# Performance work log

Hardware: AMD Instinct MI355X
Metric: run time of the kernel (lower is better)

Reference implementation:

```python
import jax, jax.numpy as jnp
import numpy as np

L = 2        # layer_depth
H = 128      # rnn_size (== embedding dim)
V = 50257    # vocab_size
B = 100      # batch_size
T = 50       # seq_length


def setup_inputs() -> dict:
    key = jax.random.key(0)
    ks = jax.random.split(key, 8)
    inp = {
        'input_data': jax.random.randint(ks[0], (B, T), 0, V, dtype=jnp.int32),
        # embedding ~ U(-0.08, 0.08) as in the original
        'embedding': jax.random.uniform(ks[1], (V, H), jnp.float32, -0.08, 0.08),
        # per-layer GRU params; input dim == H for every layer
        'gate_k': jax.random.normal(ks[2], (L, 2 * H, 2 * H), jnp.float32) * 0.05,
        'gate_b': jnp.ones((L, 2 * H), jnp.float32),  # TF GRUCell gate bias init = 1.0
        'cand_k': jax.random.normal(ks[3], (L, 2 * H, H), jnp.float32) * 0.05,
        'cand_b': jnp.zeros((L, H), jnp.float32),
        'softmax_w': jax.random.normal(ks[4], (V, H), jnp.float32) * 0.05,
        'softmax_b': jnp.zeros((V,), jnp.float32),
    }
    return inp


def _gru_scan(x_bth, gate_k, gate_b, cand_k, cand_b):
    # x_bth: [B, T, H] embedded inputs. Stacked L-layer GRU, TF GRUCell math:
    #   r,u = sigmoid([x,h] @ Wg + bg);  c = tanh([x, r*h] @ Wc + bc)
    #   h' = u*h + (1-u)*c
    x_tbh = jnp.swapaxes(x_bth, 0, 1)  # [T, B, H]
    h0 = jnp.zeros((L, x_bth.shape[0], H), x_bth.dtype)

    def step(hs, x_t):
        inp = x_t
        new_hs = []
        for l in range(L):
            h = hs[l]
            g = jax.nn.sigmoid(jnp.concatenate([inp, h], -1) @ gate_k[l] + gate_b[l])
            r, u = g[:, :H], g[:, H:]
            c = jnp.tanh(jnp.concatenate([inp, r * h], -1) @ cand_k[l] + cand_b[l])
            h_new = u * h + (1.0 - u) * c
            new_hs.append(h_new)
            inp = h_new
        return jnp.stack(new_hs), inp

    final_state, out_tbh = jax.lax.scan(step, h0, x_tbh)
    return jnp.swapaxes(out_tbh, 0, 1), final_state  # [B, T, H], [L, B, H]


def reference(input_data, embedding, gate_k, gate_b, cand_k, cand_b, softmax_w, softmax_b):
    x = embedding[input_data]                                   # [B, T, H]
    out, _ = _gru_scan(x, gate_k, gate_b, cand_k, cand_b)       # [B, T, H]
    out = out.reshape(-1, H)                                    # [B*T, H]
    logits = out @ softmax_w.T + softmax_b                      # [B*T, V]
    probs = jax.nn.softmax(logits, axis=-1)
    return logits, probs
```

## Files before the change

kernel.cpp:

```cpp
#include <hip/hip_runtime.h>
#include <hip/hip_bf16.h>
#include <math.h>

#define GL 2
#define GH 128
#define GH2 256
#define GV 50257
#define GB 100
#define GT 50
#define GM 5000
#define NT 393
#define MT 40

typedef __attribute__((ext_vector_type(4))) float f32x4;
typedef __attribute__((ext_vector_type(8))) short bf16x8;

__global__ __launch_bounds__(1024) void gru_kernel(
    const int* __restrict__ tok,
    const float* __restrict__ emb,
    const float* __restrict__ gate_k,
    const float* __restrict__ gate_b,
    const float* __restrict__ cand_k,
    const float* __restrict__ cand_b,
    float* __restrict__ out)
{
    const int b = blockIdx.x;
    const int tid = threadIdx.x;

    __shared__ float xin[GH2];
    __shared__ float hs[2][GH];
    __shared__ float g[GH2];
    __shared__ float gpart[4][GH2];
    __shared__ float cpart[8][GH];

    if (tid < GH) { hs[0][tid] = 0.f; hs[1][tid] = 0.f; }
    __syncthreads();

    for (int t = 0; t < GT; ++t) {
        const int token = tok[b * GT + t];
        if (tid < GH) xin[tid] = emb[(size_t)token * GH + tid];

        for (int l = 0; l < GL; ++l) {
            if (tid >= GH && tid < GH2) xin[tid] = hs[l][tid - GH];
            __syncthreads();

            {
                const int j  = tid & 255;
                const int t4 = tid >> 8;
                const float* gcol = gate_k + (size_t)l * GH2 * GH2 + (size_t)(t4 * 64) * GH2 + j;
                const float* xv = xin + t4 * 64;
                float acc = 0.f;
                #pragma unroll 16
                for (int i = 0; i < 64; ++i) acc += xv[i] * gcol[(size_t)i * GH2];
                gpart[t4][j] = acc;
            }
            __syncthreads();
            if (tid < GH2) {
                float s = gpart[0][tid] + gpart[1][tid] + gpart[2][tid] + gpart[3][tid]
                        + gate_b[l * GH2 + tid];
                g[tid] = 1.f / (1.f + expf(-s));
            }
            __syncthreads();
            if (tid >= GH && tid < GH2) xin[tid] = g[tid - GH] * hs[l][tid - GH];
            __syncthreads();

            {
                const int j  = tid & 127;
                const int t8 = tid >> 7;
                const float* ccol = cand_k + (size_t)l * GH2 * GH + (size_t)(t8 * 32) * GH + j;
                const float* xv = xin + t8 * 32;
                float acc = 0.f;
                #pragma unroll 16
                for (int i = 0; i < 32; ++i) acc += xv[i] * ccol[(size_t)i * GH];
                cpart[t8][j] = acc;
            }
            __syncthreads();
            if (tid < GH) {
                float csum = 0.f;
                #pragma unroll
                for (int p = 0; p < 8; ++p) csum += cpart[p][tid];
                const float c = tanhf(csum + cand_b[l * GH + tid]);
                const float u = g[GH + tid];
                const float hn = u * hs[l][tid] + (1.f - u) * c;
                hs[l][tid] = hn;
                xin[tid] = hn;
                if (l == GL - 1) out[(size_t)(b * GT + t) * GH + tid] = hn;
            }
            __syncthreads();
        }
    }
}

__device__ __forceinline__ unsigned short f2bf(float x) {
    union { float f; unsigned u; } c; c.f = x;
    unsigned r = c.u + 0x7FFFu + ((c.u >> 16) & 1u);
    return (unsigned short)(r >> 16);
}
__device__ __forceinline__ float bf2f(unsigned short b) {
    union { unsigned u; float f; } c; c.u = ((unsigned)b) << 16; return c.f;
}

__global__ __launch_bounds__(256) void prep_kernel(
    const float* __restrict__ src, unsigned short* __restrict__ dst,
    int ntiles, int nrows)
{
    const int idx = blockIdx.x * 256 + threadIdx.x;
    if (idx >= ntiles * 4 * 128) return;
    const int r    = idx & 127;
    const int c    = idx >> 7;
    const int cs   = c & 3;
    const int tile = c >> 2;
    int row = tile * 128 + r; if (row > nrows - 1) row = nrows - 1;
    const float* s = src + (size_t)row * GH + (cs & 1) * 64;
    unsigned short* d = dst + (size_t)c * 8192 + r * 64;
    const bool lo = (cs >= 2);
    const int rx = r & 7;

    #pragma unroll
    for (int gq = 0; gq < 8; ++gq) {
        float x[8];
        *(float4*)(x)     = *(const float4*)(s + gq * 8);
        *(float4*)(x + 4) = *(const float4*)(s + gq * 8 + 4);
        unsigned u[4];
        #pragma unroll
        for (int q = 0; q < 4; ++q) {
            const float a0 = x[q * 2], a1 = x[q * 2 + 1];
            const unsigned short hi0 = f2bf(a0), hi1 = f2bf(a1);
            unsigned short h0, h1;
            if (lo) { h0 = f2bf(a0 - bf2f(hi0)); h1 = f2bf(a1 - bf2f(hi1)); }
            else    { h0 = hi0; h1 = hi1; }
            u[q] = (unsigned)h0 | ((unsigned)h1 << 16);
        }
        *(uint4*)(d + (size_t)((gq ^ rx) * 8)) = *(const uint4*)u;
    }
}

__global__ __launch_bounds__(256) void mfma_logits_kernel(
    const unsigned short* __restrict__ Ap, const unsigned short* __restrict__ Wp,
    const float* __restrict__ bias,
    float* __restrict__ logits, float* __restrict__ pmax, float* __restrict__ psum)
{
    __shared__ unsigned short ldsA[8192];
    __shared__ unsigned short ldsW[8192];
    __shared__ float sM[2][128];
    __shared__ float sS[2][128];

    const int bt  = blockIdx.x;
    const int bm  = blockIdx.y;
    const int tid = threadIdx.x;
    const int wid  = tid >> 6;
    const int lane = tid & 63;
    const int wm = wid >> 1, wn = wid & 1;
    const int l15 = lane & 15, l4 = lane >> 4;

    f32x4 acc[4][4];
    #pragma unroll
    for (int i = 0; i < 4; ++i)
        #pragma unroll
        for (int j = 0; j < 4; ++j) acc[i][j] = (f32x4){0.f, 0.f, 0.f, 0.f};

    #pragma unroll
    for (int s = 0; s < 6; ++s) {
        const int ac = (s < 2) ? s : (s < 4) ? (s - 2) : (s - 2);
        const int wc = (s < 4) ? s : (s - 4);
        const unsigned short* ga = Ap + (size_t)(bm * 4 + ac) * 8192 + wid * 2048 + lane * 8;
        const unsigned short* gw = Wp + (size_t)(bt * 4 + wc) * 8192 + wid * 2048 + lane * 8;
        #pragma unroll
        for (int i = 0; i < 4; ++i)
            __builtin_amdgcn_global_load_lds(
                (const __attribute__((address_space(1))) void*)(ga + i * 512),
                (__attribute__((address_space(3))) void*)(&ldsA[wid * 2048 + i * 512]), 16, 0, 0);
        #pragma unroll
        for (int i = 0; i < 4; ++i)
            __builtin_amdgcn_global_load_lds(
                (const __attribute__((address_space(1))) void*)(gw + i * 512),
                (__attribute__((address_space(3))) void*)(&ldsW[wid * 2048 + i * 512]), 16, 0, 0);
        __syncthreads();

        #pragma unroll
        for (int ks = 0; ks < 2; ++ks) {
            bf16x8 af[4], bf[4];
            #pragma unroll
            for (int mi = 0; mi < 4; ++mi) {
                const int row = wm * 64 + mi * 16 + l15;
                const int off = row * 64 + ((ks * 32 + l4 * 8) ^ ((row & 7) << 3));
                af[mi] = *(const bf16x8*)&ldsA[off];
            }
            #pragma unroll
            for (int nj = 0; nj < 4; ++nj) {
                const int row = wn * 64 + nj * 16 + l15;
                const int off = row * 64 + ((ks * 32 + l4 * 8) ^ ((row & 7) << 3));
                bf[nj] = *(const bf16x8*)&ldsW[off];
            }
            #pragma unroll
            for (int mi = 0; mi < 4; ++mi)
                #pragma unroll
                for (int nj = 0; nj < 4; ++nj)
                    acc[mi][nj] = __builtin_amdgcn_mfma_f32_16x16x32_bf16(
                        af[mi], bf[nj], acc[mi][nj], 0, 0, 0);
        }
        __syncthreads();
    }

    float bj[4]; bool nv[4];
    #pragma unroll
    for (int nj = 0; nj < 4; ++nj) {
        const int n = bt * 128 + wn * 64 + nj * 16 + l15;
        nv[nj] = (n < GV);
        bj[nj] = nv[nj] ? bias[n] : 0.f;
    }
    #pragma unroll
    for (int mi = 0; mi < 4; ++mi) {
        #pragma unroll
        for (int r = 0; r < 4; ++r) {
            const int rowb = wm * 64 + mi * 16 + l4 * 4 + r;
            const int m = bm * 128 + rowb;
            float v[4];
            #pragma unroll
            for (int nj = 0; nj < 4; ++nj) v[nj] = acc[mi][nj][r] + bj[nj];
            if (m < GM) {
                #pragma unroll
                for (int nj = 0; nj < 4; ++nj)
                    if (nv[nj])
                        logits[(size_t)m * GV + (bt * 128 + wn * 64 + nj * 16 + l15)] = v[nj];
            }
            float mx = -INFINITY;
            #pragma unroll
            for (int nj = 0; nj < 4; ++nj) if (nv[nj]) mx = fmaxf(mx, v[nj]);
            #pragma unroll
            for (int d = 1; d < 16; d <<= 1) mx = fmaxf(mx, __shfl_xor(mx, d));
            float se = 0.f;
            #pragma unroll
            for (int nj = 0; nj < 4; ++nj) if (nv[nj]) se += expf(v[nj] - mx);
            #pragma unroll
            for (int d = 1; d < 16; d <<= 1) se += __shfl_xor(se, d);
            if (l15 == 0) { sM[wn][rowb] = mx; sS[wn][rowb] = se; }
        }
    }
    __syncthreads();
    if (tid < 128) {
        const int m = bm * 128 + tid;
        if (m < GM) {
            const float m0 = sM[0][tid], m1 = sM[1][tid];
            const float M = fmaxf(m0, m1);
            const float S = sS[0][tid] * expf(m0 - M) + sS[1][tid] * expf(m1 - M);
            pmax[(size_t)m * NT + bt] = M;
            psum[(size_t)m * NT + bt] = S;
        }
    }
}

__global__ __launch_bounds__(64) void reduce_kernel(
    const float* __restrict__ pmax, const float* __restrict__ psum,
    float* __restrict__ rowM, float* __restrict__ rowInvS)
{
    const int m = blockIdx.x;
    const int lane = threadIdx.x;
    float M = -INFINITY, S = 0.f;
    for (int t = lane; t < NT; t += 64) {
        const float m2 = pmax[(size_t)m * NT + t];
        const float s2 = psum[(size_t)m * NT + t];
        const float nM = fmaxf(M, m2);
        S = S * expf(M - nM) + s2 * expf(m2 - nM);
        M = nM;
    }
    #pragma unroll
    for (int d = 1; d < 64; d <<= 1) {
        const float m2 = __shfl_xor(M, d);
        const float s2 = __shfl_xor(S, d);
        const float nM = fmaxf(M, m2);
        S = S * expf(M - nM) + s2 * expf(m2 - nM);
        M = nM;
    }
    if (lane == 0) { rowM[m] = M; rowInvS[m] = 1.f / S; }
}

__global__ __launch_bounds__(256) void probs_kernel(
    const float* __restrict__ logits,
    const float* __restrict__ rowM, const float* __restrict__ rowInvS,
    float* __restrict__ probs)
{
    const float4* L4 = reinterpret_cast<const float4*>(logits);
    float4* P4 = reinterpret_cast<float4*>(probs);
    const int n4 = (int)(((long long)GM * GV) / 4);
    const int stride = gridDim.x * blockDim.x;
    for (int i = blockIdx.x * blockDim.x + threadIdx.x; i < n4; i += stride) {
        const float4 v = L4[i];
        const int base = i * 4;
        const int m0 = base / GV;
        const int m3 = (base + 3) / GV;
        float4 o;
        if (m0 == m3) {
            const float M = rowM[m0], Is = rowInvS[m0];
            o.x = expf(v.x - M) * Is;
            o.y = expf(v.y - M) * Is;
            o.z = expf(v.z - M) * Is;
            o.w = expf(v.w - M) * Is;
        } else {
            const int ma = base / GV, mb = (base + 1) / GV;
            const int mc = (base + 2) / GV, md = (base + 3) / GV;
            o.x = expf(v.x - rowM[ma]) * rowInvS[ma];
            o.y = expf(v.y - rowM[mb]) * rowInvS[mb];
            o.z = expf(v.z - rowM[mc]) * rowInvS[mc];
            o.w = expf(v.w - rowM[md]) * rowInvS[md];
        }
        P4[i] = o;
    }
}

extern "C" void kernel_launch(void* const* d_in, const int* in_sizes, int n_in,
                              void* d_out, int out_size, void* d_ws, size_t ws_size,
                              hipStream_t stream) {
    const int*   tok    = (const int*)d_in[0];
    const float* emb    = (const float*)d_in[1];
    const float* gate_k = (const float*)d_in[2];
    const float* gate_b = (const float*)d_in[3];
    const float* cand_k = (const float*)d_in[4];
    const float* cand_b = (const float*)d_in[5];
    const float* W      = (const float*)d_in[6];
    const float* bias   = (const float*)d_in[7];

    float* logits = (float*)d_out;
    float* probs  = logits + (size_t)GM * GV;

    float* ws = (float*)d_ws;
    float* gruout = ws;
    unsigned short* Ap = (unsigned short*)(gruout + 640000);
    unsigned short* Wp = Ap + (size_t)MT * 4 * 8192;
    float* pmax    = (float*)(Wp + (size_t)NT * 4 * 8192);
    float* psum    = pmax + (size_t)GM * NT;
    float* rowM    = psum + (size_t)GM * NT;
    float* rowInvS = rowM + GM;

    gru_kernel<<<GB, 1024, 0, stream>>>(tok, emb, gate_k, gate_b, cand_k, cand_b, gruout);

    prep_kernel<<<(MT * 4 * 128 + 255) / 256, 256, 0, stream>>>(gruout, Ap, MT, GM);
    prep_kernel<<<(NT * 4 * 128 + 255) / 256, 256, 0, stream>>>(W, Wp, NT, GV);

    dim3 g2(NT, MT);
    mfma_logits_kernel<<<g2, 256, 0, stream>>>(Ap, Wp, bias, logits, pmax, psum);

    reduce_kernel<<<GM, 64, 0, stream>>>(pmax, psum, rowM, rowInvS);

    probs_kernel<<<2048, 256, 0, stream>>>(logits, rowM, rowInvS, probs);
}
```

Before: 1.429 ms.

## Batch four sequences per GRU block, double-buffer logits LDS, use fast exp

The GRU kernel now handles four batch rows per 1024-thread block. Each weight load is reused across four accumulators, and the block count drops from 100 to 25. The MFMA logits kernel double-buffers its A/W LDS tiles so the next stage's global-to-LDS loads are issued while the current stage computes. Softmax exponentials switch to __expf, and the probs kernel grid is doubled. The risks are lower parallelism in the serial GRU, more LDS per logits block, and slightly reduced exp accuracy.

After: 1.672 ms. +17.0%, slower.

```diff
diff --git a/kernel.cpp b/kernel.cpp
--- a/kernel.cpp
+++ b/kernel.cpp
@@ -11,6 +11,7 @@
 #define GM 5000
 #define NT 393
 #define MT 40
+#define BPB 4
 
 typedef __attribute__((ext_vector_type(4))) float f32x4;
 typedef __attribute__((ext_vector_type(8))) short bf16x8;
@@ -24,67 +25,83 @@
     const float* __restrict__ cand_b,
     float* __restrict__ out)
 {
-    const int b = blockIdx.x;
+    const int b0 = blockIdx.x * BPB;
     const int tid = threadIdx.x;
 
-    __shared__ float xin[GH2];
-    __shared__ float hs[2][GH];
-    __shared__ float g[GH2];
-    __shared__ float gpart[4][GH2];
-    __shared__ float cpart[8][GH];
-
-    if (tid < GH) { hs[0][tid] = 0.f; hs[1][tid] = 0.f; }
+    __shared__ float xin[BPB][GH2];
+    __shared__ float hs[GL][BPB][GH];
+    __shared__ float g[BPB][GH2];
+    __shared__ float gpart[4][BPB][GH2];
+    __shared__ float cpart[8][BPB][GH];
+
+    for (int i = tid; i < GL * BPB * GH; i += 1024) ((float*)hs)[i] = 0.f;
     __syncthreads();
 
     for (int t = 0; t < GT; ++t) {
-        const int token = tok[b * GT + t];
-        if (tid < GH) xin[tid] = emb[(size_t)token * GH + tid];
-
+        if (tid < BPB * GH) {
+            const int bb = tid >> 7, d = tid & 127;
+            const int token = tok[(b0 + bb) * GT + t];
+            xin[bb][d] = emb[(size_t)token * GH + d];
+        }
         for (int l = 0; l < GL; ++l) {
-            if (tid >= GH && tid < GH2) xin[tid] = hs[l][tid - GH];
+            if (tid < BPB * GH) {
+                const int bb = tid >> 7, d = tid & 127;
+                xin[bb][GH + d] = hs[l][bb][d];
+            }
             __syncthreads();
 
             {
-                const int j  = tid & 255;
-                const int t4 = tid >> 8;
+                const int j = tid & 255, t4 = tid >> 8;
                 const float* gcol = gate_k + (size_t)l * GH2 * GH2 + (size_t)(t4 * 64) * GH2 + j;
-                const float* xv = xin + t4 * 64;
-                float acc = 0.f;
-                #pragma unroll 16
-                for (int i = 0; i < 64; ++i) acc += xv[i] * gcol[(size_t)i * GH2];
-                gpart[t4][j] = acc;
-            }
-            __syncthreads();
-            if (tid < GH2) {
-                float s = gpart[0][tid] + gpart[1][tid] + gpart[2][tid] + gpart[3][tid]
-                        + gate_b[l * GH2 + tid];
-                g[tid] = 1.f / (1.f + expf(-s));
-            }
-            __syncthreads();
-            if (tid >= GH && tid < GH2) xin[tid] = g[tid - GH] * hs[l][tid - GH];
-            __syncthreads();
-
+                float acc[BPB] = {0.f, 0.f, 0.f, 0.f};
+                #pragma unroll 8
+                for (int i = 0; i < 64; ++i) {
+                    const float w = gcol[(size_t)i * GH2];
+                    #pragma unroll
+                    for (int bb = 0; bb < BPB; ++bb) acc[bb] += xin[bb][t4 * 64 + i] * w;
+                }
+                #pragma unroll
+                for (int bb = 0; bb < BPB; ++bb) gpart[t4][bb][j] = acc[bb];
+            }
+            __syncthreads();
             {
-                const int j  = tid & 127;
-                const int t8 = tid >> 7;
+                const int bb = tid >> 8, j = tid & 255;
+                const float s = gpart[0][bb][j] + gpart[1][bb][j] + gpart[2][bb][j]
+                              + gpart[3][bb][j] + gate_b[l * GH2 + j];
+                g[bb][j] = 1.f / (1.f + __expf(-s));
+            }
+            __syncthreads();
+            if (tid < BPB * GH) {
+                const int bb = tid >> 7, d = tid & 127;
+                xin[bb][GH + d] = g[bb][d] * hs[l][bb][d];
+            }
+            __syncthreads();
+
+            {
+                const int j = tid & 127, t8 = tid >> 7;
                 const float* ccol = cand_k + (size_t)l * GH2 * GH + (size_t)(t8 * 32) * GH + j;
-                const float* xv = xin + t8 * 32;
-                float acc = 0.f;
-                #pragma unroll 16
-                for (int i = 0; i < 32; ++i) acc += xv[i] * ccol[(size_t)i * GH];
-                cpart[t8][j] = acc;
-            }
-            __syncthreads();
-            if (tid < GH) {
+                float acc[BPB] = {0.f, 0.f, 0.f, 0.f};
+                #pragma unroll 8
+                for (int i = 0; i < 32; ++i) {
+                    const float w = ccol[(size_t)i * GH];
+                    #pragma unroll
+                    for (int bb = 0; bb < BPB; ++bb) acc[bb] += xin[bb][t8 * 32 + i] * w;
+                }
+                #pragma unroll
+                for (int bb = 0; bb < BPB; ++bb) cpart[t8][bb][j] = acc[bb];
+            }
+            __syncthreads();
+            if (tid < BPB * GH) {
+                const int bb = tid >> 7, d = tid & 127;
                 float csum = 0.f;
                 #pragma unroll
-                for (int p = 0; p < 8; ++p) csum += cpart[p][tid];
-                const float c = tanhf(csum + cand_b[l * GH + tid]);
-                const float u = g[GH + tid];
-                const float hn = u * hs[l][tid] + (1.f - u) * c;
-                hs[l][tid] = hn;
-                xin[tid] = hn;
-                if (l == GL - 1) out[(size_t)(b * GT + t) * GH + tid] = hn;
+                for (int p = 0; p < 8; ++p) csum += cpart[p][bb][d];
+                const float c = tanhf(csum + cand_b[l * GH + d]);
+                const float u = g[bb][GH + d];
+                const float hn = u * hs[l][bb][d] + (1.f - u) * c;
+                hs[l][bb][d] = hn;
+                xin[bb][d] = hn;
+                if (l == GL - 1) out[(size_t)((b0 + bb) * GT + t) * GH + d] = hn;
             }
             __syncthreads();
         }
@@ -140,8 +157,8 @@
     const float* __restrict__ bias,
     float* __restrict__ logits, float* __restrict__ pmax, float* __restrict__ psum)
 {
-    __shared__ unsigned short ldsA[8192];
-    __shared__ unsigned short ldsW[8192];
+    __shared__ unsigned short ldsA[2][8192];
+    __shared__ unsigned short ldsW[2][8192];
     __shared__ float sM[2][128];
     __shared__ float sS[2][128];
 
@@ -153,29 +170,38 @@
     const int wm = wid >> 1, wn = wid & 1;
     const int l15 = lane & 15, l4 = lane >> 4;
 
+    constexpr int amap[6] = {0, 1, 0, 1, 2, 3};
+    constexpr int wmap[6] = {0, 1, 2, 3, 0, 1};
+
     f32x4 acc[4][4];
     #pragma unroll
     for (int i = 0; i < 4; ++i)
         #pragma unroll
         for (int j = 0; j < 4; ++j) acc[i][j] = (f32x4){0.f, 0.f, 0.f, 0.f};
 
+#define STAGE(BUF, S)                                                                   \
+    {                                                                                   \
+        const unsigned short* ga = Ap + (size_t)(bm * 4 + amap[S]) * 8192 + wid * 2048 + lane * 8; \
+        const unsigned short* gw = Wp + (size_t)(bt * 4 + wmap[S]) * 8192 + wid * 2048 + lane * 8; \
+        _Pragma("unroll")                                                               \
+        for (int i = 0; i < 4; ++i)                                                     \
+            __builtin_amdgcn_global_load_lds(                                           \
+                (const __attribute__((address_space(1))) void*)(ga + i * 512),          \
+                (__attribute__((address_space(3))) void*)(&ldsA[BUF][wid * 2048 + i * 512]), 16, 0, 0); \
+        _Pragma("unroll")                                                               \
+        for (int i = 0; i < 4; ++i)                                                     \
+            __builtin_amdgcn_global_load_lds(                                           \
+                (const __attribute__((address_space(1))) void*)(gw + i * 512),          \
+                (__attribute__((address_space(3))) void*)(&ldsW[BUF][wid * 2048 + i * 512]), 16, 0, 0); \
+    }
+
+    STAGE(0, 0);
+    __syncthreads();
+
     #pragma unroll
     for (int s = 0; s < 6; ++s) {
-        const int ac = (s < 2) ? s : (s < 4) ? (s - 2) : (s - 2);
-        const int wc = (s < 4) ? s : (s - 4);
-        const unsigned short* ga = Ap + (size_t)(bm * 4 + ac) * 8192 + wid * 2048 + lane * 8;
-        const unsigned short* gw = Wp + (size_t)(bt * 4 + wc) * 8192 + wid * 2048 + lane * 8;
-        #pragma unroll
-        for (int i = 0; i < 4; ++i)
-            __builtin_amdgcn_global_load_lds(
-                (const __attribute__((address_space(1))) void*)(ga + i * 512),
-                (__attribute__((address_space(3))) void*)(&ldsA[wid * 2048 + i * 512]), 16, 0, 0);
-        #pragma unroll
-        for (int i = 0; i < 4; ++i)
-            __builtin_amdgcn_global_load_lds(
-                (const __attribute__((address_space(1))) void*)(gw + i * 512),
-                (__attribute__((address_space(3))) void*)(&ldsW[wid * 2048 + i * 512]), 16, 0, 0);
-        __syncthreads();
+        const int cur = s & 1;
+        if (s < 5) STAGE(s ^ 1 ? (s + 1) & 1 : (s + 1) & 1, s + 1);
 
         #pragma unroll
         for (int ks = 0; ks < 2; ++ks) {
@@ -184,13 +210,13 @@
             for (int mi = 0; mi < 4; ++mi) {
                 const int row = wm * 64 + mi * 16 + l15;
                 const int off = row * 64 + ((ks * 32 + l4 * 8) ^ ((row & 7) << 3));
-                af[mi] = *(const bf16x8*)&ldsA[off];
+                af[mi] = *(const bf16x8*)&ldsA[cur][off];
             }
             #pragma unroll
             for (int nj = 0; nj < 4; ++nj) {
                 const int row = wn * 64 + nj * 16 + l15;
                 const int off = row * 64 + ((ks * 32 + l4 * 8) ^ ((row & 7) << 3));
-                bf[nj] = *(const bf16x8*)&ldsW[off];
+                bf[nj] = *(const bf16x8*)&ldsW[cur][off];
             }
             #pragma unroll
             for (int mi = 0; mi < 4; ++mi)
@@ -201,6 +227,7 @@
         }
         __syncthreads();
     }
+#undef STAGE
 
     float bj[4]; bool nv[4];
     #pragma unroll
@@ -231,7 +258,7 @@
             for (int d = 1; d < 16; d <<= 1) mx = fmaxf(mx, __shfl_xor(mx, d));
             float se = 0.f;
             #pragma unroll
-            for (int nj = 0; nj < 4; ++nj) if (nv[nj]) se += expf(v[nj] - mx);
+            for (int nj = 0; nj < 4; ++nj) if (nv[nj]) se += __expf(v[nj] - mx);
             #pragma unroll
             for (int d = 1; d < 16; d <<= 1) se += __shfl_xor(se, d);
             if (l15 == 0) { sM[wn][rowb] = mx; sS[wn][rowb] = se; }
@@ -243,7 +270,7 @@
         if (m < GM) {
             const float m0 = sM[0][tid], m1 = sM[1][tid];
             const float M = fmaxf(m0, m1);
-            const float S = sS[0][tid] * expf(m0 - M) + sS[1][tid] * expf(m1 - M);
+            const float S = sS[0][tid] * __expf(m0 - M) + sS[1][tid] * __expf(m1 - M);
             pmax[(size_t)m * NT + bt] = M;
             psum[(size_t)m * NT + bt] = S;
         }
@@ -292,17 +319,17 @@
         float4 o;
         if (m0 == m3) {
             const float M = rowM[m0], Is = rowInvS[m0];
-            o.x = expf(v.x - M) * Is;
-            o.y = expf(v.y - M) * Is;
-            o.z = expf(v.z - M) * Is;
-            o.w = expf(v.w - M) * Is;
+            o.x = __expf(v.x - M) * Is;
+            o.y = __expf(v.y - M) * Is;
+            o.z = __expf(v.z - M) * Is;
+            o.w = __expf(v.w - M) * Is;
         } else {
             const int ma = base / GV, mb = (base + 1) / GV;
             const int mc = (base + 2) / GV, md = (base + 3) / GV;
-            o.x = expf(v.x - rowM[ma]) * rowInvS[ma];
-            o.y = expf(v.y - rowM[mb]) * rowInvS[mb];
-            o.z = expf(v.z - rowM[mc]) * rowInvS[mc];
-            o.w = expf(v.w - rowM[md]) * rowInvS[md];
+            o.x = __expf(v.x - rowM[ma]) * rowInvS[ma];
+            o.y = __expf(v.y - rowM[mb]) * rowInvS[mb];
+            o.z = __expf(v.z - rowM[mc]) * rowInvS[mc];
+            o.w = __expf(v.w - rowM[md]) * rowInvS[md];
         }
         P4[i] = o;
     }
@@ -332,7 +359,7 @@
     float* rowM    = psum + (size_t)GM * NT;
     float* rowInvS = rowM + GM;
 
-    gru_kernel<<<GB, 1024, 0, stream>>>(tok, emb, gate_k, gate_b, cand_k, cand_b, gruout);
+    gru_kernel<<<GB / BPB, 1024, 0, stream>>>(tok, emb, gate_k, gate_b, cand_k, cand_b, gruout);
 
     prep_kernel<<<(MT * 4 * 128 + 255) / 256, 256, 0, stream>>>(gruout, Ap, MT, GM);
     prep_kernel<<<(NT * 4 * 128 + 255) / 256, 256, 0, stream>>>(W, Wp, NT, GV);
@@ -342,5 +369,5 @@
 
     reduce_kernel<<<GM, 64, 0, stream>>>(pmax, psum, rowM, rowInvS);
 
-    probs_kernel<<<2048, 256, 0, stream>>>(logits, rowM, rowInvS, probs);
-}
+    probs_kernel<<<4096, 256, 0, stream>>>(logits, rowM, rowInvS, probs);
+}
```
